# Kernel optimization log

Hardware: AMD Instinct MI355X
Metric: run time of the kernel (lower is better)

The kernel has to match this reference:

```python
import jax, jax.numpy as jnp
import numpy as np

N = 100000
HEADS = 4
NHID = 32


def _gat_conv(x, src, dst, W, a_src, a_dst, b):
    # x: [N, Fin]; src/dst: [E'] (self-loops already appended)
    h = (x @ W).reshape(N, HEADS, NHID)                      # [N, H, D]
    al_src = jnp.einsum('nhd,hd->nh', h, a_src)              # [N, H]
    al_dst = jnp.einsum('nhd,hd->nh', h, a_dst)
    e = jax.nn.leaky_relu(al_src[src] + al_dst[dst], 0.2)    # [E', H]
    # segment softmax over incoming edges of each destination node
    m = jax.ops.segment_max(e, dst, num_segments=N)          # [N, H]
    ex = jnp.exp(e - m[dst])
    s = jax.ops.segment_sum(ex, dst, num_segments=N)         # [N, H]
    alpha = ex / (s[dst] + 1e-16)                            # [E', H]
    msg = h[src] * alpha[:, :, None]                         # [E', H, D]
    out = jax.ops.segment_sum(msg, dst, num_segments=N)      # [N, H, D]
    return out.reshape(N, HEADS * NHID) + b


def setup_inputs() -> dict:
    key = jax.random.key(0)
    ks = jax.random.split(key, 16)
    E = 1600000
    NFEAT, NCLASS = 128, 10
    width = HEADS * NHID  # 128
    sc = 0.1
    inp = {
        'x': jax.random.normal(ks[0], (N, NFEAT), jnp.float32),
        'edge_index': jax.random.randint(ks[1], (2, E), 0, N, jnp.int64)
            if jax.config.jax_enable_x64 else jax.random.randint(ks[1], (2, E), 0, N, jnp.int32),
        'W0': jax.random.normal(ks[2], (NFEAT, width), jnp.float32) * sc,
        'a_src0': jax.random.normal(ks[3], (HEADS, NHID), jnp.float32) * sc,
        'a_dst0': jax.random.normal(ks[4], (HEADS, NHID), jnp.float32) * sc,
        'b0': jnp.zeros((width,), jnp.float32),
        'W1': jax.random.normal(ks[5], (width, width), jnp.float32) * sc,
        'a_src1': jax.random.normal(ks[6], (HEADS, NHID), jnp.float32) * sc,
        'a_dst1': jax.random.normal(ks[7], (HEADS, NHID), jnp.float32) * sc,
        'b1': jnp.zeros((width,), jnp.float32),
        'W2': jax.random.normal(ks[8], (width, width), jnp.float32) * sc,
        'a_src2': jax.random.normal(ks[9], (HEADS, NHID), jnp.float32) * sc,
        'a_dst2': jax.random.normal(ks[10], (HEADS, NHID), jnp.float32) * sc,
        'b2': jnp.zeros((width,), jnp.float32),
        'fc_W': jax.random.normal(ks[11], (width, NCLASS), jnp.float32) * sc,
        'fc_b': jnp.zeros((NCLASS,), jnp.float32),
    }
    return inp


def reference(x, edge_index, W0, a_src0, a_dst0, b0, W1, a_src1, a_dst1, b1,
              W2, a_src2, a_dst2, b2, fc_W, fc_b):
    # PyG GATConv default add_self_loops=True
    loops = jnp.arange(N, dtype=edge_index.dtype)
    src = jnp.concatenate([edge_index[0], loops])
    dst = jnp.concatenate([edge_index[1], loops])
    h = x
    for (W, a_s, a_d, b) in ((W0, a_src0, a_dst0, b0),
                             (W1, a_src1, a_dst1, b1),
                             (W2, a_src2, a_dst2, b2)):
        h = jax.nn.elu(_gat_conv(h, src, dst, W, a_s, a_d, b))
        # F.dropout(training=False) -> identity
    logits = h @ fc_W + fc_b
    return jax.nn.log_softmax(logits, axis=1)
```

## Files before the change

### kernel.cpp

```cpp
#include <hip/hip_runtime.h>
#include <math.h>

#define NN 100000
#define FEAT 128
#define NHEAD 4
#define BSH 9
#define BNODES 512
#define NBUCK 196
#define BCAP 16384
#define PA_EPT 16
#define GTILES 6250

typedef unsigned int uint;
typedef unsigned short ushort;
typedef __attribute__((ext_vector_type(8))) short short8;
typedef __attribute__((ext_vector_type(4))) float fx4;

__device__ __forceinline__ float lrelu(float v) { return v > 0.f ? v : 0.2f * v; }

__device__ __forceinline__ ushort f2bf(float f) {
    uint u = __float_as_uint(f);
    return (ushort)((u + 0x7fffu + ((u >> 16) & 1u)) >> 16);
}
__device__ __forceinline__ float bf_lo(uint u) { return __uint_as_float(u << 16); }
__device__ __forceinline__ float bf_hi(uint u) { return __uint_as_float(u & 0xffff0000u); }

__global__ __launch_bounds__(256) void convert_bf_kernel(
    const float* __restrict__ x, ushort* __restrict__ xbf)
{
    int i = blockIdx.x * 256 + threadIdx.x;
    if (i >= NN * FEAT / 4) return;
    float4 v = ((const float4*)x)[i];
    ushort4 u;
    u.x = f2bf(v.x); u.y = f2bf(v.y); u.z = f2bf(v.z); u.w = f2bf(v.w);
    ((ushort4*)xbf)[i] = u;
}

__global__ __launch_bounds__(256, 2) void gemm_mfma_kernel(
    const ushort* __restrict__ inbf, const float* __restrict__ W,
    const float* __restrict__ a_src, const float* __restrict__ a_dst,
    ushort* __restrict__ hbf, float* __restrict__ al_s, float* __restrict__ al_d)
{
    __shared__ __align__(16) ushort WA[FEAT * FEAT];
    const int t = threadIdx.x;
    for (int idx = t; idx < FEAT * FEAT; idx += 256) {
        int k = idx >> 7, m = idx & 127;
        int mt = m >> 4, kt = k >> 5, qq = (k >> 3) & 3, j = k & 7;
        int ln = qq * 16 + (m & 15);
        WA[((mt * 4 + kt) * 64 + ln) * 8 + j] = f2bf(W[idx]);
    }
    __syncthreads();

    const int wv = t >> 6, lane = t & 63;
    const int node_l = lane & 15, q = lane >> 4;

    short8 afr[8][4];
    #pragma unroll
    for (int mt = 0; mt < 8; ++mt)
        #pragma unroll
        for (int kt = 0; kt < 4; ++kt)
            afr[mt][kt] = *(const short8*)&WA[((mt * 4 + kt) * 64 + lane) * 8];

    for (int tile = blockIdx.x * 4 + wv; tile < GTILES; tile += gridDim.x * 4) {
        const int n0 = tile * 16;
        const ushort* rowp = inbf + (size_t)(n0 + node_l) * FEAT + q * 8;
        short8 b0 = *(const short8*)(rowp);
        short8 b1 = *(const short8*)(rowp + 32);
        short8 b2 = *(const short8*)(rowp + 64);
        short8 b3 = *(const short8*)(rowp + 96);
        fx4 zero = {0.f, 0.f, 0.f, 0.f};
        fx4 acc[8];
        #pragma unroll
        for (int mt = 0; mt < 8; ++mt) acc[mt] = zero;
        #pragma unroll
        for (int kt = 0; kt < 4; ++kt) {
            short8 b = (kt == 0) ? b0 : (kt == 1) ? b1 : (kt == 2) ? b2 : b3;
            #pragma unroll
            for (int mt = 0; mt < 8; ++mt)
                acc[mt] = __builtin_amdgcn_mfma_f32_16x16x32_bf16(afr[mt][kt], b, acc[mt], 0, 0, 0);
        }
        float ps[4] = {0.f, 0.f, 0.f, 0.f};
        float pd[4] = {0.f, 0.f, 0.f, 0.f};
        #pragma unroll
        for (int mt = 0; mt < 8; ++mt) {
            float4 as4 = *(const float4*)(a_src + mt * 16 + q * 4);
            float4 ad4 = *(const float4*)(a_dst + mt * 16 + q * 4);
            ps[mt >> 1] += acc[mt][0] * as4.x + acc[mt][1] * as4.y + acc[mt][2] * as4.z + acc[mt][3] * as4.w;
            pd[mt >> 1] += acc[mt][0] * ad4.x + acc[mt][1] * ad4.y + acc[mt][2] * ad4.z + acc[mt][3] * ad4.w;
            ushort4 hv;
            hv.x = f2bf(acc[mt][0]); hv.y = f2bf(acc[mt][1]);
            hv.z = f2bf(acc[mt][2]); hv.w = f2bf(acc[mt][3]);
            *(ushort4*)(hbf + (size_t)(n0 + node_l) * FEAT + mt * 16 + q * 4) = hv;
        }
        #pragma unroll
        for (int h = 0; h < 4; ++h) {
            ps[h] += __shfl_xor(ps[h], 16); ps[h] += __shfl_xor(ps[h], 32);
            pd[h] += __shfl_xor(pd[h], 16); pd[h] += __shfl_xor(pd[h], 32);
        }
        float vs = (q == 0) ? ps[0] : (q == 1) ? ps[1] : (q == 2) ? ps[2] : ps[3];
        float vd = (q == 0) ? pd[0] : (q == 1) ? pd[1] : (q == 2) ? pd[2] : pd[3];
        al_s[(n0 + node_l) * 4 + q] = vs;
        al_d[(n0 + node_l) * 4 + q] = vd;
    }
}


__global__ void zero_small_kernel(int* bsize)
{
    int t = threadIdx.x;
    if (t < NBUCK) bsize[t] = 0;
}

__global__ __launch_bounds__(256) void bucket_hist_kernel(
    const int* __restrict__ ei, int E, int* bsize)
{
    __shared__ int lh[NBUCK];
    int t = threadIdx.x;
    if (t < NBUCK) lh[t] = 0;
    __syncthreads();
    int stride = gridDim.x * 256;
    for (int i = blockIdx.x * 256 + t; i < E + NN; i += stride) {
        int d = (i < E) ? ei[E + i] : (i - E);
        atomicAdd(&lh[d >> BSH], 1);
    }
    __syncthreads();
    if (t < NBUCK && lh[t]) atomicAdd(&bsize[t], lh[t]);
}

__global__ void bucket_scan_kernel(const int* __restrict__ bsize, int* bbase, int* bcursor)
{
    if (threadIdx.x == 0) {
        int acc = 0;
        for (int b = 0; b < NBUCK; ++b) { bbase[b] = acc; bcursor[b] = acc; acc += bsize[b]; }
        bbase[NBUCK] = acc;
    }
}

__global__ __launch_bounds__(256) void phaseA_bin_kernel(
    const int* __restrict__ ei, int E, int* bcursor, int2* __restrict__ pairs)
{
    __shared__ int lh[NBUCK], lb[NBUCK];
    int t = threadIdx.x;
    if (t < NBUCK) lh[t] = 0;
    __syncthreads();
    int base = blockIdx.x * (256 * PA_EPT) + t;
    int s[PA_EPT], d[PA_EPT];
    #pragma unroll
    for (int k = 0; k < PA_EPT; ++k) {
        int i = base + k * 256;
        if (i < E)            { s[k] = ei[i]; d[k] = ei[E + i]; }
        else if (i < E + NN)  { s[k] = i - E; d[k] = s[k]; }
        else                  { s[k] = 0; d[k] = -1; }
        if (d[k] >= 0) atomicAdd(&lh[d[k] >> BSH], 1);
    }
    __syncthreads();
    if (t < NBUCK) {
        int c = lh[t];
        lb[t] = c ? atomicAdd(&bcursor[t], c) : 0;
        lh[t] = 0;
    }
    __syncthreads();
    #pragma unroll
    for (int k = 0; k < PA_EPT; ++k) {
        if (d[k] >= 0) {
            int b = d[k] >> BSH;
            int off = atomicAdd(&lh[b], 1);
            pairs[lb[b] + off] = make_int2(d[k], s[k]);
        }
    }
}

__global__ __launch_bounds__(256) void phaseB_kernel(
    const int2* __restrict__ pairs, const int* __restrict__ bbase,
    int* __restrict__ row_ptr, int* __restrict__ colidx, int EP)
{
    __shared__ int nh[BNODES];
    __shared__ int ex[BNODES];
    __shared__ int ss[256];
    __shared__ int img[BCAP];
    int b = blockIdx.x, t = threadIdx.x;
    int node0 = b << BSH;
    int nend = min(NN - node0, BNODES);
    int pb = bbase[b], pe = bbase[b + 1];
    int span = pe - pb;
    for (int j = t; j < BNODES; j += 256) nh[j] = 0;
    __syncthreads();
    for (int i = t; i < span; i += 256)
        atomicAdd(&nh[pairs[pb + i].x - node0], 1);
    __syncthreads();
    int v0 = nh[2 * t], v1 = nh[2 * t + 1];
    int psc = v0 + v1;
    ss[t] = psc;
    __syncthreads();
    #pragma unroll
    for (int off = 1; off < 256; off <<= 1) {
        int x = (t >= off) ? ss[t - off] : 0;
        __syncthreads();
        ss[t] += x;
        __syncthreads();
    }
    int ep = ss[t] - psc;
    ex[2 * t] = ep;
    ex[2 * t + 1] = ep + v0;
    __syncthreads();
    for (int j = t; j < nend; j += 256) row_ptr[node0 + j] = pb + ex[j];
    if (b == NBUCK - 1 && t == 0) row_ptr[NN] = EP;
    for (int j = t; j < BNODES; j += 256) nh[j] = ex[j];
    __syncthreads();
    if (span <= BCAP) {
        for (int i = t; i < span; i += 256) {
            int2 p = pairs[pb + i];
            int pos = atomicAdd(&nh[p.x - node0], 1);
            img[pos] = p.y;
        }
        __syncthreads();
        for (int i = t; i < span; i += 256) colidx[pb + i] = img[i];
    } else {
        for (int i = t; i < span; i += 256) {
            int2 p = pairs[pb + i];
            int pos = atomicAdd(&nh[p.x - node0], 1);
            colidx[pb + pos] = p.y;
        }
    }
}

#define AGGR_STEP(hv, wgt)                                                    \
    a0 = fmaf(wgt, bf_lo(hv.x), a0); a1 = fmaf(wgt, bf_hi(hv.x), a1);        \
    a2 = fmaf(wgt, bf_lo(hv.y), a2); a3 = fmaf(wgt, bf_hi(hv.y), a3);        \
    a4 = fmaf(wgt, bf_lo(hv.z), a4); a5 = fmaf(wgt, bf_hi(hv.z), a5);        \
    a6 = fmaf(wgt, bf_lo(hv.w), a6); a7 = fmaf(wgt, bf_hi(hv.w), a7);

__global__ __launch_bounds__(256) void aggr_csr_kernel(
    const int* __restrict__ row_ptr, const int* __restrict__ colidx,
    const ushort* __restrict__ hbf, const float* __restrict__ al_s,
    const float* __restrict__ al_d, const float* __restrict__ bias,
    ushort* __restrict__ outbf)
{
    int t = threadIdx.x;
    int node = blockIdx.x * 16 + (t >> 4);
    if (node >= NN) return;
    int lane = t & 15;
    int head = lane >> 2;
    float ald_h = al_d[node * 4 + head];
    int beg = row_ptr[node], end = row_ptr[node + 1];

    float ssum = 0.f;
    float a0=0.f,a1=0.f,a2=0.f,a3=0.f,a4=0.f,a5=0.f,a6=0.f,a7=0.f;

    int p = beg;
    for (; p + 8 <= end; p += 8) {
        int s0 = colidx[p],   s1 = colidx[p+1], s2 = colidx[p+2], s3 = colidx[p+3];
        int s4 = colidx[p+4], s5 = colidx[p+5], s6 = colidx[p+6], s7 = colidx[p+7];
        float w0 = __expf(lrelu(al_s[s0*4 + head] + ald_h));
        float w1 = __expf(lrelu(al_s[s1*4 + head] + ald_h));
        float w2 = __expf(lrelu(al_s[s2*4 + head] + ald_h));
        float w3 = __expf(lrelu(al_s[s3*4 + head] + ald_h));
        float w4 = __expf(lrelu(al_s[s4*4 + head] + ald_h));
        float w5 = __expf(lrelu(al_s[s5*4 + head] + ald_h));
        float w6 = __expf(lrelu(al_s[s6*4 + head] + ald_h));
        float w7 = __expf(lrelu(al_s[s7*4 + head] + ald_h));
        uint4 h0 = ((const uint4*)(hbf + (size_t)s0 * FEAT))[lane];
        uint4 h1 = ((const uint4*)(hbf + (size_t)s1 * FEAT))[lane];
        uint4 h2 = ((const uint4*)(hbf + (size_t)s2 * FEAT))[lane];
        uint4 h3 = ((const uint4*)(hbf + (size_t)s3 * FEAT))[lane];
        uint4 h4 = ((const uint4*)(hbf + (size_t)s4 * FEAT))[lane];
        uint4 h5 = ((const uint4*)(hbf + (size_t)s5 * FEAT))[lane];
        uint4 h6 = ((const uint4*)(hbf + (size_t)s6 * FEAT))[lane];
        uint4 h7 = ((const uint4*)(hbf + (size_t)s7 * FEAT))[lane];
        ssum += ((w0 + w1) + (w2 + w3)) + ((w4 + w5) + (w6 + w7));
        AGGR_STEP(h0, w0) AGGR_STEP(h1, w1) AGGR_STEP(h2, w2) AGGR_STEP(h3, w3)
        AGGR_STEP(h4, w4) AGGR_STEP(h5, w5) AGGR_STEP(h6, w6) AGGR_STEP(h7, w7)
    }
    for (; p + 4 <= end; p += 4) {
        int s0 = colidx[p], s1 = colidx[p+1], s2 = colidx[p+2], s3 = colidx[p+3];
        float w0 = __expf(lrelu(al_s[s0*4 + head] + ald_h));
        float w1 = __expf(lrelu(al_s[s1*4 + head] + ald_h));
        float w2 = __expf(lrelu(al_s[s2*4 + head] + ald_h));
        float w3 = __expf(lrelu(al_s[s3*4 + head] + ald_h));
        uint4 h0 = ((const uint4*)(hbf + (size_t)s0 * FEAT))[lane];
        uint4 h1 = ((const uint4*)(hbf + (size_t)s1 * FEAT))[lane];
        uint4 h2 = ((const uint4*)(hbf + (size_t)s2 * FEAT))[lane];
        uint4 h3 = ((const uint4*)(hbf + (size_t)s3 * FEAT))[lane];
        ssum += (w0 + w1) + (w2 + w3);
        AGGR_STEP(h0, w0) AGGR_STEP(h1, w1) AGGR_STEP(h2, w2) AGGR_STEP(h3, w3)
    }
    for (; p < end; ++p) {
        int sn = colidx[p];
        float wq = __expf(lrelu(al_s[sn*4 + head] + ald_h));
        uint4 hv = ((const uint4*)(hbf + (size_t)sn * FEAT))[lane];
        ssum += wq;
        AGGR_STEP(hv, wq)
    }
    float inv = 1.f / (ssum + 1e-16f);
    const float* bp = bias + lane * 8;
    float o[8] = {a0,a1,a2,a3,a4,a5,a6,a7};
    #pragma unroll
    for (int k = 0; k < 8; ++k) {
        float v = o[k] * inv + bp[k];
        o[k] = v > 0.f ? v : __expf(v) - 1.f;
    }
    uint4 u;
    u.x = (uint)f2bf(o[0]) | ((uint)f2bf(o[1]) << 16);
    u.y = (uint)f2bf(o[2]) | ((uint)f2bf(o[3]) << 16);
    u.z = (uint)f2bf(o[4]) | ((uint)f2bf(o[5]) << 16);
    u.w = (uint)f2bf(o[6]) | ((uint)f2bf(o[7]) << 16);
    ((uint4*)(outbf + (size_t)node * FEAT))[lane] = u;
}

__global__ __launch_bounds__(256) void fc_kernel(
    const ushort* __restrict__ hbf, const float* __restrict__ fcW,
    const float* __restrict__ fcb, float* __restrict__ out)
{
    __shared__ float WT[10][FEAT];
    __shared__ float bl[10];
    int t = threadIdx.x;
    for (int i = t; i < FEAT * 10; i += 256) {
        int k = i / 10, c = i % 10;
        WT[c][k] = fcW[i];
    }
    if (t < 10) bl[t] = fcb[t];
    __syncthreads();
    int n = blockIdx.x * 256 + t;
    if (n >= NN) return;
    const uint4* row = (const uint4*)(hbf + (size_t)n * FEAT);
    float lg[10];
    #pragma unroll
    for (int c = 0; c < 10; ++c) lg[c] = bl[c];
    #pragma unroll 4
    for (int k8 = 0; k8 < 16; ++k8) {
        uint4 u = row[k8];
        float x0 = bf_lo(u.x), x1 = bf_hi(u.x), x2 = bf_lo(u.y), x3 = bf_hi(u.y);
        float x4 = bf_lo(u.z), x5 = bf_hi(u.z), x6 = bf_lo(u.w), x7 = bf_hi(u.w);
        #pragma unroll
        for (int c = 0; c < 10; ++c) {
            const float* wr = &WT[c][k8 * 8];
            float4 wa = *(const float4*)(wr);
            float4 wb = *(const float4*)(wr + 4);
            float acc = fmaf(x0, wa.x, fmaf(x1, wa.y, fmaf(x2, wa.z, x3 * wa.w)));
            acc = fmaf(x4, wb.x, fmaf(x5, wb.y, fmaf(x6, wb.z, fmaf(x7, wb.w, acc))));
            lg[c] += acc;
        }
    }
    float mx = lg[0];
    #pragma unroll
    for (int c = 1; c < 10; ++c) mx = fmaxf(mx, lg[c]);
    float se = 0.f;
    #pragma unroll
    for (int c = 0; c < 10; ++c) se += __expf(lg[c] - mx);
    float lse = mx + __logf(se);
    float2* op = (float2*)(out + (size_t)n * 10);
    #pragma unroll
    for (int c = 0; c < 5; ++c)
        op[c] = make_float2(lg[2*c] - lse, lg[2*c + 1] - lse);
}

extern "C" void kernel_launch(void* const* d_in, const int* in_sizes, int n_in,
                              void* d_out, int out_size, void* d_ws, size_t ws_size,
                              hipStream_t stream)
{
    const float* x   = (const float*)d_in[0];
    const int*   ei  = (const int*)d_in[1];
    const float* W[3]   = {(const float*)d_in[2], (const float*)d_in[6],  (const float*)d_in[10]};
    const float* asr[3] = {(const float*)d_in[3], (const float*)d_in[7],  (const float*)d_in[11]};
    const float* ads[3] = {(const float*)d_in[4], (const float*)d_in[8],  (const float*)d_in[12]};
    const float* bs[3]  = {(const float*)d_in[5], (const float*)d_in[9],  (const float*)d_in[13]};
    const float* fcW = (const float*)d_in[14];
    const float* fcb = (const float*)d_in[15];
    const int E  = in_sizes[1] / 2;
    const int EP = E + NN;

    ushort* xbf  = (ushort*)d_ws;
    ushort* hbf  = xbf + (size_t)NN * FEAT;
    ushort* ybf  = hbf + (size_t)NN * FEAT;
    float* als   = (float*)(ybf + (size_t)NN * FEAT);
    float* ald   = als + (size_t)NN * NHEAD;
    int* row_ptr = (int*)(ald + (size_t)NN * NHEAD);
    int* bsize   = row_ptr + NN + 1;
    int* bbase   = bsize + NBUCK;
    int* bcursor = bbase + NBUCK + 1;
    int2* pairs  = (int2*)(bcursor + NBUCK);
    int* colidx  = (int*)(pairs + (size_t)EP);

    zero_small_kernel<<<1, 256, 0, stream>>>(bsize);
    bucket_hist_kernel<<<1024, 256, 0, stream>>>(ei, E, bsize);
    bucket_scan_kernel<<<1, 64, 0, stream>>>(bsize, bbase, bcursor);
    phaseA_bin_kernel<<<(EP + 256*PA_EPT - 1) / (256*PA_EPT), 256, 0, stream>>>(ei, E, bcursor, pairs);
    phaseB_kernel<<<NBUCK, 256, 0, stream>>>(pairs, bbase, row_ptr, colidx, EP);

    convert_bf_kernel<<<(NN * FEAT / 4 + 255) / 256, 256, 0, stream>>>(x, xbf);

    const ushort* fin = xbf;
    for (int l = 0; l < 3; ++l) {
        gemm_mfma_kernel<<<512, 256, 0, stream>>>(fin, W[l], asr[l], ads[l], hbf, als, ald);
        aggr_csr_kernel<<<(NN + 15) / 16, 256, 0, stream>>>(row_ptr, colidx, hbf, als, ald, bs[l], ybf);
        fin = ybf;
    }
    fc_kernel<<<(NN + 255) / 256, 256, 0, stream>>>(ybf, fcW, fcb, (float*)d_out);
}
```

Baseline: 509.6 us.

## Prefetch next GEMM tile, read A fragments from LDS, vectorize CSR index loads

The GEMM kernel now builds the bf16 W fragments in LDS with per-lane short8 stores. It reads those fragments from LDS inside the MFMA loop instead of holding 32 short8 registers per lane. This frees registers so the launch bound can allow 4 blocks per CU and the grid doubles to 1024. It also software-prefetches the next tile's input row while computing the current one. The aggregation kernel drops its 8-wide unroll for 4-wide steps that load column indices as int4 and prefetch the next int4. The trade-off is fewer independent gathers in flight per step, and an int4 load from an arbitrary CSR offset that may not be 16-byte aligned.

New measurement: 679.7 us. 33.4% more time.

```diff
diff --git a/kernel.cpp b/kernel.cpp
--- a/kernel.cpp
+++ b/kernel.cpp
@@ -36,38 +36,53 @@
     ((ushort4*)xbf)[i] = u;
 }
 
-__global__ __launch_bounds__(256, 2) void gemm_mfma_kernel(
+__global__ __launch_bounds__(256, 4) void gemm_mfma_kernel(
     const ushort* __restrict__ inbf, const float* __restrict__ W,
     const float* __restrict__ a_src, const float* __restrict__ a_dst,
     ushort* __restrict__ hbf, float* __restrict__ al_s, float* __restrict__ al_d)
 {
     __shared__ __align__(16) ushort WA[FEAT * FEAT];
     const int t = threadIdx.x;
-    for (int idx = t; idx < FEAT * FEAT; idx += 256) {
-        int k = idx >> 7, m = idx & 127;
-        int mt = m >> 4, kt = k >> 5, qq = (k >> 3) & 3, j = k & 7;
-        int ln = qq * 16 + (m & 15);
-        WA[((mt * 4 + kt) * 64 + ln) * 8 + j] = f2bf(W[idx]);
-    }
-    __syncthreads();
-
     const int wv = t >> 6, lane = t & 63;
+    {
+        int ln = lane;
+        int mm15 = ln & 15, qq = ln >> 4;
+        for (int f = wv; f < 32; f += 4) {
+            int mt = f >> 2, kt = f & 3;
+            int m = mt * 16 + mm15;
+            int kb = kt * 32 + qq * 8;
+            short8 v;
+            #pragma unroll
+            for (int j = 0; j < 8; ++j)
+                v[j] = (short)f2bf(W[(kb + j) * FEAT + m]);
+            *(short8*)&WA[(f * 64 + ln) * 8] = v;
+        }
+    }
+    __syncthreads();
+
     const int node_l = lane & 15, q = lane >> 4;
-
-    short8 afr[8][4];
-    #pragma unroll
-    for (int mt = 0; mt < 8; ++mt)
-        #pragma unroll
-        for (int kt = 0; kt < 4; ++kt)
-            afr[mt][kt] = *(const short8*)&WA[((mt * 4 + kt) * 64 + lane) * 8];
-
-    for (int tile = blockIdx.x * 4 + wv; tile < GTILES; tile += gridDim.x * 4) {
+    const int stride = gridDim.x * 4;
+
+    int tile = blockIdx.x * 4 + wv;
+    if (tile >= GTILES) return;
+
+    const ushort* rowp = inbf + (size_t)(tile * 16 + node_l) * FEAT + q * 8;
+    short8 b0 = *(const short8*)(rowp);
+    short8 b1 = *(const short8*)(rowp + 32);
+    short8 b2 = *(const short8*)(rowp + 64);
+    short8 b3 = *(const short8*)(rowp + 96);
+
+    for (; tile < GTILES; tile += stride) {
         const int n0 = tile * 16;
-        const ushort* rowp = inbf + (size_t)(n0 + node_l) * FEAT + q * 8;
-        short8 b0 = *(const short8*)(rowp);
-        short8 b1 = *(const short8*)(rowp + 32);
-        short8 b2 = *(const short8*)(rowp + 64);
-        short8 b3 = *(const short8*)(rowp + 96);
+        int ntile = tile + stride;
+        short8 nb0, nb1, nb2, nb3;
+        if (ntile < GTILES) {
+            const ushort* nrp = inbf + (size_t)(ntile * 16 + node_l) * FEAT + q * 8;
+            nb0 = *(const short8*)(nrp);
+            nb1 = *(const short8*)(nrp + 32);
+            nb2 = *(const short8*)(nrp + 64);
+            nb3 = *(const short8*)(nrp + 96);
+        }
         fx4 zero = {0.f, 0.f, 0.f, 0.f};
         fx4 acc[8];
         #pragma unroll
@@ -76,8 +91,10 @@
         for (int kt = 0; kt < 4; ++kt) {
             short8 b = (kt == 0) ? b0 : (kt == 1) ? b1 : (kt == 2) ? b2 : b3;
             #pragma unroll
-            for (int mt = 0; mt < 8; ++mt)
-                acc[mt] = __builtin_amdgcn_mfma_f32_16x16x32_bf16(afr[mt][kt], b, acc[mt], 0, 0, 0);
+            for (int mt = 0; mt < 8; ++mt) {
+                short8 a = *(const short8*)&WA[((mt * 4 + kt) * 64 + lane) * 8];
+                acc[mt] = __builtin_amdgcn_mfma_f32_16x16x32_bf16(a, b, acc[mt], 0, 0, 0);
+            }
         }
         float ps[4] = {0.f, 0.f, 0.f, 0.f};
         float pd[4] = {0.f, 0.f, 0.f, 0.f};
@@ -101,6 +118,7 @@
         float vd = (q == 0) ? pd[0] : (q == 1) ? pd[1] : (q == 2) ? pd[2] : pd[3];
         al_s[(n0 + node_l) * 4 + q] = vs;
         al_d[(n0 + node_l) * 4 + q] = vd;
+        b0 = nb0; b1 = nb1; b2 = nb2; b3 = nb3;
     }
 }
 
@@ -230,6 +248,21 @@
     a4 = fmaf(wgt, bf_lo(hv.z), a4); a5 = fmaf(wgt, bf_hi(hv.z), a5);        \
     a6 = fmaf(wgt, bf_lo(hv.w), a6); a7 = fmaf(wgt, bf_hi(hv.w), a7);
 
+#define PROC4(cv)                                                             \
+    {                                                                         \
+        int s0 = cv.x, s1 = cv.y, s2 = cv.z, s3 = cv.w;                       \
+        float w0 = __expf(lrelu(al_s[s0*4 + head] + ald_h));                  \
+        float w1 = __expf(lrelu(al_s[s1*4 + head] + ald_h));                  \
+        float w2 = __expf(lrelu(al_s[s2*4 + head] + ald_h));                  \
+        float w3 = __expf(lrelu(al_s[s3*4 + head] + ald_h));                  \
+        uint4 h0 = ((const uint4*)(hbf + (size_t)s0 * FEAT))[lane];           \
+        uint4 h1 = ((const uint4*)(hbf + (size_t)s1 * FEAT))[lane];           \
+        uint4 h2 = ((const uint4*)(hbf + (size_t)s2 * FEAT))[lane];           \
+        uint4 h3 = ((const uint4*)(hbf + (size_t)s3 * FEAT))[lane];           \
+        ssum += (w0 + w1) + (w2 + w3);                                        \
+        AGGR_STEP(h0, w0) AGGR_STEP(h1, w1) AGGR_STEP(h2, w2) AGGR_STEP(h3, w3) \
+    }
+
 __global__ __launch_bounds__(256) void aggr_csr_kernel(
     const int* __restrict__ row_ptr, const int* __restrict__ colidx,
     const ushort* __restrict__ hbf, const float* __restrict__ al_s,
@@ -248,42 +281,15 @@
     float a0=0.f,a1=0.f,a2=0.f,a3=0.f,a4=0.f,a5=0.f,a6=0.f,a7=0.f;
 
     int p = beg;
-    for (; p + 8 <= end; p += 8) {
-        int s0 = colidx[p],   s1 = colidx[p+1], s2 = colidx[p+2], s3 = colidx[p+3];
-        int s4 = colidx[p+4], s5 = colidx[p+5], s6 = colidx[p+6], s7 = colidx[p+7];
-        float w0 = __expf(lrelu(al_s[s0*4 + head] + ald_h));
-        float w1 = __expf(lrelu(al_s[s1*4 + head] + ald_h));
-        float w2 = __expf(lrelu(al_s[s2*4 + head] + ald_h));
-        float w3 = __expf(lrelu(al_s[s3*4 + head] + ald_h));
-        float w4 = __expf(lrelu(al_s[s4*4 + head] + ald_h));
-        float w5 = __expf(lrelu(al_s[s5*4 + head] + ald_h));
-        float w6 = __expf(lrelu(al_s[s6*4 + head] + ald_h));
-        float w7 = __expf(lrelu(al_s[s7*4 + head] + ald_h));
-        uint4 h0 = ((const uint4*)(hbf + (size_t)s0 * FEAT))[lane];
-        uint4 h1 = ((const uint4*)(hbf + (size_t)s1 * FEAT))[lane];
-        uint4 h2 = ((const uint4*)(hbf + (size_t)s2 * FEAT))[lane];
-        uint4 h3 = ((const uint4*)(hbf + (size_t)s3 * FEAT))[lane];
-        uint4 h4 = ((const uint4*)(hbf + (size_t)s4 * FEAT))[lane];
-        uint4 h5 = ((const uint4*)(hbf + (size_t)s5 * FEAT))[lane];
-        uint4 h6 = ((const uint4*)(hbf + (size_t)s6 * FEAT))[lane];
-        uint4 h7 = ((const uint4*)(hbf + (size_t)s7 * FEAT))[lane];
-        ssum += ((w0 + w1) + (w2 + w3)) + ((w4 + w5) + (w6 + w7));
-        AGGR_STEP(h0, w0) AGGR_STEP(h1, w1) AGGR_STEP(h2, w2) AGGR_STEP(h3, w3)
-        AGGR_STEP(h4, w4) AGGR_STEP(h5, w5) AGGR_STEP(h6, w6) AGGR_STEP(h7, w7)
-    }
-    for (; p + 4 <= end; p += 4) {
-        int s0 = colidx[p], s1 = colidx[p+1], s2 = colidx[p+2], s3 = colidx[p+3];
-        float w0 = __expf(lrelu(al_s[s0*4 + head] + ald_h));
-        float w1 = __expf(lrelu(al_s[s1*4 + head] + ald_h));
-        float w2 = __expf(lrelu(al_s[s2*4 + head] + ald_h));
-        float w3 = __expf(lrelu(al_s[s3*4 + head] + ald_h));
-        uint4 h0 = ((const uint4*)(hbf + (size_t)s0 * FEAT))[lane];
-        uint4 h1 = ((const uint4*)(hbf + (size_t)s1 * FEAT))[lane];
-        uint4 h2 = ((const uint4*)(hbf + (size_t)s2 * FEAT))[lane];
-        uint4 h3 = ((const uint4*)(hbf + (size_t)s3 * FEAT))[lane];
-        ssum += (w0 + w1) + (w2 + w3);
-        AGGR_STEP(h0, w0) AGGR_STEP(h1, w1) AGGR_STEP(h2, w2) AGGR_STEP(h3, w3)
-    }
+    int4 ca;
+    if (p + 4 <= end) ca = *(const int4*)&colidx[p];
+    while (p + 8 <= end) {
+        int4 na = *(const int4*)&colidx[p + 4];
+        PROC4(ca)
+        ca = na;
+        p += 4;
+    }
+    if (p + 4 <= end) { PROC4(ca) p += 4; }
     for (; p < end; ++p) {
         int sn = colidx[p];
         float wq = __expf(lrelu(al_s[sn*4 + head] + ald_h));
@@ -391,7 +397,7 @@
 
     const ushort* fin = xbf;
     for (int l = 0; l < 3; ++l) {
-        gemm_mfma_kernel<<<512, 256, 0, stream>>>(fin, W[l], asr[l], ads[l], hbf, als, ald);
+        gemm_mfma_kernel<<<1024, 256, 0, stream>>>(fin, W[l], asr[l], ads[l], hbf, als, ald);
         aggr_csr_kernel<<<(NN + 15) / 16, 256, 0, stream>>>(row_ptr, colidx, hbf, als, ald, bs[l], ybf);
         fin = ybf;
     }
```
